# Performance work log

Hardware: AMD Instinct MI355X
Metric: run time of the kernel (lower is better)

## Reference

```python
import jax, jax.numpy as jnp
import numpy as np

WS = 3          # window_size == patch size (asserted in the torch forward)
R = WS // 2
V = WS ** 3     # 27 voxels per patch == window length
D_MODEL = 256
HEADS = 8
LAYERS = 3

_IDX = np.arange(WS)[:, None] + np.arange(WS)[None, :]  # [WS, WS] sliding-window indices into padded grid


def _layer_norm(x, g, b, eps=1e-5):
    mu = jnp.mean(x, axis=-1, keepdims=True)
    var = jnp.var(x, axis=-1, keepdims=True)
    return (x - mu) * jax.lax.rsqrt(var + eps) * g + b


def _gather_windows(x):
    # x: [B, WS, WS, WS, C] -> zero-padded 3x3x3 neighborhoods, [B*V, V, C]
    xp = jnp.pad(x, ((0, 0), (R, R), (R, R), (R, R), (0, 0)))
    nb = xp[:, _IDX][:, :, :, _IDX][:, :, :, :, :, _IDX]
    # axes: [B, d_ctr, d_win, h_ctr, h_win, w_ctr, w_win, C]
    nb = nb.transpose(0, 1, 3, 5, 2, 4, 6, 7)
    return nb.reshape(x.shape[0] * V, V, x.shape[-1])


def _window_mask(known_mask):
    # boundary (padding) positions -> False; interior -> known_mask value
    mp = jnp.pad(known_mask, ((0, 0), (R, R), (R, R), (R, R)))
    m = mp[:, _IDX][:, :, :, _IDX][:, :, :, :, :, _IDX]
    m = m.transpose(0, 1, 3, 5, 2, 4, 6)
    return m.reshape(known_mask.shape[0] * V, V)


def _forward(neighbors_patch, known_mask, w_in, b_in, pos_embed,
             ln1_g, ln1_b, ln2_g, ln2_b,
             Wq, bq, Wk, bk, Wv, bv, Wo, bo,
             W1, b1, W2, b2, w_out, b_out):
    B = neighbors_patch.shape[0]
    d = w_in.shape[0]
    hd = d // HEADS
    scale = hd ** -0.5
    # Conv3d(1, d, kernel_size=1) == per-voxel affine scalar -> d channels; then +pos_embed
    x = neighbors_patch[:, 0, :, :, :, None] * w_in + b_in + pos_embed  # [B,WS,WS,WS,d]
    mask = _window_mask(known_mask)  # [B*V, V] (constant across layers)
    N = B * V
    t = x.reshape(N, d)
    for l in range(LAYERS):
        # NOTE: K/V come from RAW (un-normed) neighbor embeddings, Q from norm1(target) - as in the torch code
        nb = _gather_windows(t.reshape(B, WS, WS, WS, d))  # [N, V, d]
        tn = _layer_norm(t, ln1_g[l], ln1_b[l])
        q = (tn @ Wq[l] + bq[l]).reshape(N, HEADS, hd)
        k = (nb @ Wk[l] + bk[l]).reshape(N, V, HEADS, hd)
        v = (nb @ Wv[l] + bv[l]).reshape(N, V, HEADS, hd)
        s = jnp.einsum('nhd,nlhd->nhl', q, k) * scale
        s = jnp.where(mask[:, None, :], s, -1e30)
        # fully-masked rows: torch softmax gives NaN then zeroed; here uniform*mask -> 0, same result
        a = jax.nn.softmax(s, axis=-1) * mask[:, None, :]
        o = jnp.einsum('nhl,nlhd->nhd', a, v).reshape(N, d) @ Wo[l] + bo[l]
        t = t + o  # dropout is identity in eval
        tn2 = _layer_norm(t, ln2_g[l], ln2_b[l])
        h = jax.nn.gelu(tn2 @ W1[l] + b1[l], approximate=False)
        t = t + h @ W2[l] + b2[l]
    center = t.reshape(B, WS, WS, WS, d)[:, R, R, R, :]
    return (center @ w_out)[:, None] + b_out  # [B, 1]


def setup_inputs():
    key = jax.random.key(0)
    ks = jax.random.split(key, 24)
    B, d, L, ff = 256, D_MODEL, LAYERS, 4 * D_MODEL
    nrm = lambda k, shape, s=0.02: jax.random.normal(k, shape, jnp.float32) * s
    return {
        'neighbors_patch': (jax.random.uniform(ks[0], (B, 1, WS, WS, WS)) < 0.5).astype(jnp.float32),
        'known_mask': jax.random.randint(ks[1], (B, WS, WS, WS), 0, 2).astype(bool),
        'w_in': nrm(ks[2], (d,), 0.5), 'b_in': nrm(ks[3], (d,)),
        'pos_embed': nrm(ks[4], (WS, WS, WS, d)),
        'ln1_g': jnp.ones((L, d)), 'ln1_b': jnp.zeros((L, d)),
        'ln2_g': jnp.ones((L, d)), 'ln2_b': jnp.zeros((L, d)),
        'Wq': nrm(ks[5], (L, d, d)), 'bq': nrm(ks[6], (L, d)),
        'Wk': nrm(ks[7], (L, d, d)), 'bk': nrm(ks[8], (L, d)),
        'Wv': nrm(ks[9], (L, d, d)), 'bv': nrm(ks[10], (L, d)),
        'Wo': nrm(ks[11], (L, d, d)), 'bo': nrm(ks[12], (L, d)),
        'W1': nrm(ks[13], (L, d, ff)), 'b1': nrm(ks[14], (L, ff)),
        'W2': nrm(ks[15], (L, ff, d)), 'b2': nrm(ks[16], (L, d)),
        'w_out': nrm(ks[17], (d,)), 'b_out': nrm(ks[18], (1,)),
    }


def reference(neighbors_patch, known_mask, w_in, b_in, pos_embed, ln1_g, ln1_b, ln2_g, ln2_b, Wq, bq, Wk, bk, Wv, bv, Wo, bo, W1, b1, W2, b2, w_out, b_out):
    return _forward(neighbors_patch, known_mask, w_in, b_in, pos_embed, ln1_g, ln1_b, ln2_g, ln2_b, Wq, bq, Wk, bk, Wv, bv, Wo, bo, W1, b1, W2, b2, w_out, b_out)
```

## Files before the change

kernel.cpp:

```cpp
#include <hip/hip_runtime.h>
#include <hip/hip_bf16.h>


#define NTOK 6912
#define DM   256
#define FF   1024

typedef __hip_bfloat16 bf16;
typedef __bf16 bf16x8 __attribute__((ext_vector_type(8)));
typedef float  f32x4  __attribute__((ext_vector_type(4)));

__device__ __forceinline__ void gload_lds16(const void* g, void* l) {
    __builtin_amdgcn_global_load_lds(
        (const __attribute__((address_space(1))) void*)g,
        (__attribute__((address_space(3))) void*)l, 16, 0, 0);
}

__device__ __forceinline__ unsigned short f2bf_bits(float x) {
    bf16 h = __float2bfloat16(x);
    union { bf16 h; unsigned short u; } c; c.h = h; return c.u;
}

__global__ __launch_bounds__(256) void embed_kernel(
    const float* __restrict__ npat, const float* __restrict__ w_in,
    const float* __restrict__ b_in, const float* __restrict__ pos,
    float* __restrict__ t, bf16* __restrict__ t_bf)
{
    int n = blockIdx.x;
    int c = threadIdx.x;
    int p = n % 27;
    float v = npat[n] * w_in[c] + b_in[c] + pos[p * DM + c];
    t[(size_t)n * DM + c] = v;
    t_bf[(size_t)n * DM + c] = __float2bfloat16(v);
}

__global__ void make_mask_kernel(const int* __restrict__ km,
                                 unsigned int* __restrict__ mask27)
{
    int n = blockIdx.x * blockDim.x + threadIdx.x;
    if (n >= NTOK) return;
    int b = n / 27, q = n % 27;
    int zq = q / 9, yq = (q / 3) % 3, xq = q % 3;
    unsigned int mb = 0u;
    for (int m = 0; m < 27; ++m) {
        int zm = m / 9, ym = (m / 3) % 3, xm = m % 3;
        if (abs(zm - zq) <= 1 && abs(ym - yq) <= 1 && abs(xm - xq) <= 1 &&
            km[b * 27 + m] != 0)
            mb |= (1u << m);
    }
    mask27[n] = mb;
}

__global__ __launch_bounds__(256) void convert_weights(
    const float* __restrict__ Wq, const float* __restrict__ Wk,
    const float* __restrict__ Wv, const float* __restrict__ Wo,
    const float* __restrict__ W1, const float* __restrict__ W2,
    bf16* __restrict__ Wt)
{
    __shared__ float tile[32][33];
    int id = blockIdx.z;
    int l = id / 6, wsel = id % 6;
    const float* src; bf16* dst; int K, N;
    if (wsel < 4) {
        const float* tbl[4] = {Wq, Wk, Wv, Wo};
        src = tbl[wsel] + (size_t)l * 65536; K = 256; N = 256;
        dst = Wt + (size_t)l * 786432 + wsel * 65536;
    } else if (wsel == 4) {
        src = W1 + (size_t)l * 262144; K = 256; N = 1024;
        dst = Wt + (size_t)l * 786432 + 262144;
    } else {
        src = W2 + (size_t)l * 262144; K = 1024; N = 256;
        dst = Wt + (size_t)l * 786432 + 524288;
    }
    int n0 = blockIdx.x * 32, k0 = blockIdx.y * 32;
    if (n0 >= N || k0 >= K) return;
    int tx = threadIdx.x, ty = threadIdx.y;
#pragma unroll
    for (int i = 0; i < 4; ++i)
        tile[ty + i * 8][tx] = src[(size_t)(k0 + ty + i * 8) * N + n0 + tx];
    __syncthreads();
#pragma unroll
    for (int i = 0; i < 4; ++i)
        dst[(size_t)(n0 + ty + i * 8) * K + k0 + tx] =
            __float2bfloat16(tile[tx][ty + i * 8]);
}

__global__ __launch_bounds__(256) void layernorm_kernel(
    const float* __restrict__ X, const float* __restrict__ g,
    const float* __restrict__ bta, bf16* __restrict__ Y)
{
    int n = blockIdx.x;
    int c = threadIdx.x;
    float x = X[(size_t)n * DM + c];
    float s = x, s2 = x * x;
    for (int off = 32; off; off >>= 1) {
        s  += __shfl_xor(s, off);
        s2 += __shfl_xor(s2, off);
    }
    __shared__ float ps[4], ps2[4];
    int w = c >> 6;
    if ((c & 63) == 0) { ps[w] = s; ps2[w] = s2; }
    __syncthreads();
    s  = ps[0] + ps[1] + ps[2] + ps[3];
    s2 = ps2[0] + ps2[1] + ps2[2] + ps2[3];
    float mu  = s * (1.0f / DM);
    float var = s2 * (1.0f / DM) - mu * mu;
    float r = rsqrtf(var + 1e-5f);
    Y[(size_t)n * DM + c] = __float2bfloat16((x - mu) * r * g[c] + bta[c]);
}

__device__ __forceinline__ void gemm_body(
    const bf16* __restrict__ A, const bf16* __restrict__ Bt,
    const float* __restrict__ bias, const float* __restrict__ residual,
    float* __restrict__ Cf, bf16* __restrict__ Cb,
    int K, int Nc, int act, int mode, int row0, int col0,
    bf16* As, bf16* Bs)
{
    int tid = threadIdx.x;
    int wv = tid >> 6, ln = tid & 63;
    int wr = wv >> 1, wc = wv & 1;

    f32x4 acc[4][2];
#pragma unroll
    for (int m = 0; m < 4; ++m)
#pragma unroll
        for (int n = 0; n < 2; ++n) acc[m][n] = (f32x4){0.f, 0.f, 0.f, 0.f};

    int lrow = ln >> 3;
    int kof  = (ln & 7) * 8;

    for (int k0 = 0; k0 < K; k0 += 64) {
        __syncthreads();
#pragma unroll
        for (int i = 0; i < 4; ++i) {
            int slot = i * 4 + wv;
            gload_lds16(A + (size_t)(row0 + slot * 8 + lrow) * K + k0 + kof,
                        As + slot * 512);
        }
#pragma unroll
        for (int i = 0; i < 2; ++i) {
            int slot = i * 4 + wv;
            gload_lds16(Bt + (size_t)(col0 + slot * 8 + lrow) * K + k0 + kof,
                        Bs + slot * 512);
        }
        __syncthreads();
        int lr = ln & 15, kg = ln >> 4;
#pragma unroll
        for (int kk = 0; kk < 2; ++kk) {
            int koff = kk * 32 + kg * 8;
            bf16x8 a[4], b[2];
#pragma unroll
            for (int m = 0; m < 4; ++m)
                a[m] = *(const bf16x8*)&As[(wr * 64 + m * 16 + lr) * 64 + koff];
#pragma unroll
            for (int n = 0; n < 2; ++n)
                b[n] = *(const bf16x8*)&Bs[(wc * 32 + n * 16 + lr) * 64 + koff];
#pragma unroll
            for (int m = 0; m < 4; ++m)
#pragma unroll
                for (int n = 0; n < 2; ++n)
                    acc[m][n] = __builtin_amdgcn_mfma_f32_16x16x32_bf16(
                        a[m], b[n], acc[m][n], 0, 0, 0);
        }
    }

    int lr = ln & 15, rg = ln >> 4;
#pragma unroll
    for (int m = 0; m < 4; ++m) {
#pragma unroll
        for (int n = 0; n < 2; ++n) {
            int col = col0 + wc * 32 + n * 16 + lr;
            float bcol = bias[col];
#pragma unroll
            for (int r = 0; r < 4; ++r) {
                int row = row0 + wr * 64 + m * 16 + rg * 4 + r;
                float v = acc[m][n][r] + bcol;
                if (mode == 2) {
                    int bb = row / 27, tok = row - bb * 27;
                    Cb[((size_t)bb * DM + col) * 32 + tok] = __float2bfloat16(v);
                } else {
                    size_t idx = (size_t)row * Nc + col;
                    if (residual) v += residual[idx];
                    if (act) v = 0.5f * v * (1.0f + erff(v * 0.70710678118654752f));
                    if (Cf) Cf[idx] = v;
                    if (Cb) Cb[idx] = __float2bfloat16(v);
                }
            }
        }
    }
}

__global__ __launch_bounds__(256) void gemm_bf16(
    const bf16* __restrict__ A, const bf16* __restrict__ Bt,
    const float* __restrict__ bias, const float* __restrict__ residual,
    float* __restrict__ Cf, bf16* __restrict__ Cb,
    int K, int Nc, int act)
{
    __shared__ __align__(16) bf16 As[128 * 64];
    __shared__ __align__(16) bf16 Bs[64 * 64];
    gemm_body(A, Bt, bias, residual, Cf, Cb, K, Nc, act, 0,
              blockIdx.x * 128, blockIdx.y * 64, As, Bs);
}

__global__ __launch_bounds__(256) void qkv_gemm(
    const bf16* __restrict__ tn, const bf16* __restrict__ tb,
    const bf16* __restrict__ wq,
    const float* __restrict__ bq, const float* __restrict__ bk,
    const float* __restrict__ bv,
    bf16* __restrict__ Qb, bf16* __restrict__ Kb, bf16* __restrict__ Vt)
{
    __shared__ __align__(16) bf16 As[128 * 64];
    __shared__ __align__(16) bf16 Bs[64 * 64];
    int ysel = blockIdx.y >> 2, ycol = blockIdx.y & 3;
    const bf16* A = (ysel == 0) ? tn : tb;
    const bf16* W = wq + (size_t)ysel * 65536;
    const float* bias = (ysel == 0) ? bq : (ysel == 1) ? bk : bv;
    bf16* Out = (ysel == 0) ? Qb : (ysel == 1) ? Kb : Vt;
    int mode = (ysel == 2) ? 2 : 0;
    gemm_body(A, W, bias, nullptr, nullptr, Out, DM, DM, 0, mode,
              blockIdx.x * 128, ycol * 64, As, Bs);
}

__global__ __launch_bounds__(256) void attention_mfma(
    const bf16* __restrict__ Qb, const bf16* __restrict__ Kb,
    const bf16* __restrict__ Vt, const unsigned int* __restrict__ mask27,
    bf16* __restrict__ out)
{
    __shared__ __align__(16) bf16 P_lds[4][32 * 40];
    int b  = blockIdx.x;
    int wv = threadIdx.x >> 6;
    int head = blockIdx.y * 4 + wv;
    int ln = threadIdx.x & 63;
    int r = ln & 15, g = ln >> 4;

    const bf16* Kp = Kb + (size_t)b * 27 * DM + head * 32;
    const bf16* Qp = Qb + (size_t)b * 27 * DM + head * 32;

    bf16x8 aK[2], bQ[2];
    aK[0] = *(const bf16x8*)(Kp + (size_t)r * DM + g * 8);
    aK[1] = *(const bf16x8*)(Kp + (size_t)(16 + r) * DM + g * 8);
    bQ[0] = *(const bf16x8*)(Qp + (size_t)r * DM + g * 8);
    bQ[1] = *(const bf16x8*)(Qp + (size_t)(16 + r) * DM + g * 8);

    f32x4 acc[2][2];
#pragma unroll
    for (int at = 0; at < 2; ++at)
#pragma unroll
        for (int bt = 0; bt < 2; ++bt)
            acc[at][bt] = __builtin_amdgcn_mfma_f32_16x16x32_bf16(
                aK[at], bQ[bt], (f32x4){0.f, 0.f, 0.f, 0.f}, 0, 0, 0);

    unsigned int Mq[2];
    Mq[0] = mask27[b * 27 + r];
    Mq[1] = (16 + r < 27) ? mask27[b * 27 + 16 + r] : 0u;

#pragma unroll
    for (int bt = 0; bt < 2; ++bt) {
        float e[2][4];
        float mx = -1e30f;
#pragma unroll
        for (int at = 0; at < 2; ++at)
#pragma unroll
            for (int rg = 0; rg < 4; ++rg) {
                int m = at * 16 + g * 4 + rg;
                bool in = (Mq[bt] >> m) & 1;
                float sv = acc[at][bt][rg] * 0.17677669529663687f;
                e[at][rg] = in ? sv : -1e30f;
                mx = fmaxf(mx, e[at][rg]);
            }
        mx = fmaxf(mx, __shfl_xor(mx, 16));
        mx = fmaxf(mx, __shfl_xor(mx, 32));
        float sum = 0.f;
#pragma unroll
        for (int at = 0; at < 2; ++at)
#pragma unroll
            for (int rg = 0; rg < 4; ++rg) {
                int m = at * 16 + g * 4 + rg;
                bool in = (Mq[bt] >> m) & 1;
                float ev = in ? expf(e[at][rg] - mx) : 0.f;
                e[at][rg] = ev;
                sum += ev;
            }
        sum += __shfl_xor(sum, 16);
        sum += __shfl_xor(sum, 32);
        float inv = (sum > 0.f) ? 1.f / sum : 0.f;
#pragma unroll
        for (int at = 0; at < 2; ++at) {
            ushort4 u;
            u.x = f2bf_bits(e[at][0] * inv);
            u.y = f2bf_bits(e[at][1] * inv);
            u.z = f2bf_bits(e[at][2] * inv);
            u.w = f2bf_bits(e[at][3] * inv);
            *(ushort4*)&P_lds[wv][(bt * 16 + r) * 40 + at * 16 + g * 4] = u;
        }
    }

    bf16x8 pa[2], vb[2];
    pa[0] = *(const bf16x8*)&P_lds[wv][(size_t)r * 40 + g * 8];
    pa[1] = *(const bf16x8*)&P_lds[wv][(size_t)(16 + r) * 40 + g * 8];
    const bf16* Vp = Vt + ((size_t)b * DM + head * 32) * 32;
    vb[0] = *(const bf16x8*)(Vp + (size_t)r * 32 + g * 8);
    vb[1] = *(const bf16x8*)(Vp + (size_t)(16 + r) * 32 + g * 8);

    f32x4 o[2][2];
#pragma unroll
    for (int qt = 0; qt < 2; ++qt)
#pragma unroll
        for (int dt = 0; dt < 2; ++dt)
            o[qt][dt] = __builtin_amdgcn_mfma_f32_16x16x32_bf16(
                pa[qt], vb[dt], (f32x4){0.f, 0.f, 0.f, 0.f}, 0, 0, 0);

#pragma unroll
    for (int qt = 0; qt < 2; ++qt)
#pragma unroll
        for (int dt = 0; dt < 2; ++dt)
#pragma unroll
            for (int rg = 0; rg < 4; ++rg) {
                int q = qt * 16 + g * 4 + rg;
                if (q < 27)
                    out[(size_t)(b * 27 + q) * DM + head * 32 + dt * 16 + r] =
                        __float2bfloat16(o[qt][dt][rg]);
            }
}

__global__ __launch_bounds__(256) void out_proj_kernel(
    const float* __restrict__ t, const float* __restrict__ w_out,
    const float* __restrict__ b_out, float* __restrict__ out)
{
    int bb = blockIdx.x;
    int c = threadIdx.x;
    float v = t[(size_t)(bb * 27 + 13) * DM + c] * w_out[c];
    for (int off = 32; off; off >>= 1) v += __shfl_xor(v, off);
    __shared__ float ps[4];
    if ((c & 63) == 0) ps[c >> 6] = v;
    __syncthreads();
    if (c == 0) out[bb] = ps[0] + ps[1] + ps[2] + ps[3] + b_out[0];
}

extern "C" void kernel_launch(void* const* d_in, const int* in_sizes, int n_in,
                              void* d_out, int out_size, void* d_ws, size_t ws_size,
                              hipStream_t stream)
{
    const float* npat  = (const float*)d_in[0];
    const int*   kmask = (const int*)  d_in[1];
    const float* w_in  = (const float*)d_in[2];
    const float* b_in  = (const float*)d_in[3];
    const float* pos   = (const float*)d_in[4];
    const float* ln1_g = (const float*)d_in[5];
    const float* ln1_b = (const float*)d_in[6];
    const float* ln2_g = (const float*)d_in[7];
    const float* ln2_b = (const float*)d_in[8];
    const float* Wq    = (const float*)d_in[9];
    const float* bq    = (const float*)d_in[10];
    const float* Wk    = (const float*)d_in[11];
    const float* bk    = (const float*)d_in[12];
    const float* Wv    = (const float*)d_in[13];
    const float* bv    = (const float*)d_in[14];
    const float* Wo    = (const float*)d_in[15];
    const float* bo    = (const float*)d_in[16];
    const float* W1    = (const float*)d_in[17];
    const float* b1    = (const float*)d_in[18];
    const float* W2    = (const float*)d_in[19];
    const float* b2    = (const float*)d_in[20];
    const float* w_out = (const float*)d_in[21];
    const float* b_out = (const float*)d_in[22];
    float* out = (float*)d_out;

    char* ws = (char*)d_ws;
    size_t f32mat = (size_t)NTOK * DM * 4;
    size_t bfmat  = (size_t)NTOK * DM * 2;
    float* t = (float*)(ws);
    char* p = ws + f32mat;
    bf16* t_bf   = (bf16*)(p);               p += bfmat;
    bf16* tn_bf  = (bf16*)(p);               p += bfmat;
    bf16* attn_bf= (bf16*)(p);               p += bfmat;
    bf16* Qb     = (bf16*)(p);               p += bfmat;
    bf16* Kb     = (bf16*)(p);               p += bfmat;
    bf16* Vt     = (bf16*)(p);               p += (size_t)256 * DM * 32 * 2;
    bf16* H_bf   = (bf16*)(p);               p += (size_t)NTOK * FF * 2;
    bf16* Wt     = (bf16*)(p);               p += (size_t)3 * 786432 * 2;
    unsigned int* mask27 = (unsigned int*)(p);

    convert_weights<<<dim3(32, 32, 18), dim3(32, 8), 0, stream>>>(
        Wq, Wk, Wv, Wo, W1, W2, Wt);
    embed_kernel<<<NTOK, 256, 0, stream>>>(npat, w_in, b_in, pos, t, t_bf);
    make_mask_kernel<<<(NTOK + 255) / 256, 256, 0, stream>>>(kmask, mask27);

    dim3 gDD(NTOK / 128, DM / 64);
    dim3 gQKV(NTOK / 128, 12);
    dim3 gFF(NTOK / 128, FF / 64);

    for (int l = 0; l < 3; ++l) {
        const bf16* wqt = Wt + (size_t)l * 786432;
        const bf16* wot = wqt + 3 * 65536;
        const bf16* w1t = wot + 65536;
        const bf16* w2t = w1t + 262144;

        layernorm_kernel<<<NTOK, 256, 0, stream>>>(t, ln1_g + l * DM, ln1_b + l * DM, tn_bf);
        qkv_gemm<<<gQKV, 256, 0, stream>>>(tn_bf, t_bf, wqt,
                                           bq + l * DM, bk + l * DM, bv + l * DM,
                                           Qb, Kb, Vt);
        attention_mfma<<<dim3(256, 2), 256, 0, stream>>>(Qb, Kb, Vt, mask27, attn_bf);
        gemm_bf16<<<gDD, 256, 0, stream>>>(attn_bf, wot, bo + l * DM, t, t, t_bf, DM, DM, 0);
        layernorm_kernel<<<NTOK, 256, 0, stream>>>(t, ln2_g + l * DM, ln2_b + l * DM, tn_bf);
        gemm_bf16<<<gFF, 256, 0, stream>>>(tn_bf, w1t, b1 + l * FF, nullptr, nullptr, H_bf, DM, FF, 1);
        gemm_bf16<<<gDD, 256, 0, stream>>>(H_bf, w2t, b2 + l * DM, t, t, t_bf, FF, DM, 0);
    }

    out_proj_kernel<<<256, 256, 0, stream>>>(t, w_out, b_out, out);
}
```

Before: 391.4 us.

## Double-buffer GEMM LDS tiles and fuse mask construction into embed kernel

```diff
diff --git a/kernel.cpp b/kernel.cpp
--- a/kernel.cpp
+++ b/kernel.cpp
@@ -21,34 +21,30 @@
     union { bf16 h; unsigned short u; } c; c.h = h; return c.u;
 }
 
-__global__ __launch_bounds__(256) void embed_kernel(
-    const float* __restrict__ npat, const float* __restrict__ w_in,
-    const float* __restrict__ b_in, const float* __restrict__ pos,
-    float* __restrict__ t, bf16* __restrict__ t_bf)
+__global__ __launch_bounds__(256) void embed_mask_kernel(
+    const float* __restrict__ npat, const int* __restrict__ km,
+    const float* __restrict__ w_in, const float* __restrict__ b_in,
+    const float* __restrict__ pos,
+    float* __restrict__ t, bf16* __restrict__ t_bf,
+    unsigned int* __restrict__ mask27)
 {
     int n = blockIdx.x;
     int c = threadIdx.x;
-    int p = n % 27;
-    float v = npat[n] * w_in[c] + b_in[c] + pos[p * DM + c];
+    int b = n / 27, q = n % 27;
+    float v = npat[n] * w_in[c] + b_in[c] + pos[q * DM + c];
     t[(size_t)n * DM + c] = v;
     t_bf[(size_t)n * DM + c] = __float2bfloat16(v);
-}
-
-__global__ void make_mask_kernel(const int* __restrict__ km,
-                                 unsigned int* __restrict__ mask27)
-{
-    int n = blockIdx.x * blockDim.x + threadIdx.x;
-    if (n >= NTOK) return;
-    int b = n / 27, q = n % 27;
-    int zq = q / 9, yq = (q / 3) % 3, xq = q % 3;
-    unsigned int mb = 0u;
-    for (int m = 0; m < 27; ++m) {
-        int zm = m / 9, ym = (m / 3) % 3, xm = m % 3;
-        if (abs(zm - zq) <= 1 && abs(ym - yq) <= 1 && abs(xm - xq) <= 1 &&
-            km[b * 27 + m] != 0)
-            mb |= (1u << m);
-    }
-    mask27[n] = mb;
+    if (c < 64) {
+        bool bit = false;
+        if (c < 27) {
+            int zq = q / 9, yq = (q / 3) % 3, xq = q % 3;
+            int zm = c / 9, ym = (c / 3) % 3, xm = c % 3;
+            bit = (abs(zm - zq) <= 1) && (abs(ym - yq) <= 1) &&
+                  (abs(xm - xq) <= 1) && (km[b * 27 + c] != 0);
+        }
+        unsigned long long bm = __ballot(bit);
+        if (c == 0) mask27[n] = (unsigned int)(bm & 0x7FFFFFFULL);
+    }
 }
 
 __global__ __launch_bounds__(256) void convert_weights(
@@ -128,33 +124,52 @@
 
     int lrow = ln >> 3;
     int kof  = (ln & 7) * 8;
-
-    for (int k0 = 0; k0 < K; k0 += 64) {
-        __syncthreads();
-#pragma unroll
-        for (int i = 0; i < 4; ++i) {
-            int slot = i * 4 + wv;
-            gload_lds16(A + (size_t)(row0 + slot * 8 + lrow) * K + k0 + kof,
-                        As + slot * 512);
+    int NT = K >> 6;
+
+#pragma unroll
+    for (int i = 0; i < 4; ++i) {
+        int slot = i * 4 + wv;
+        gload_lds16(A + (size_t)(row0 + slot * 8 + lrow) * K + kof,
+                    As + slot * 512);
+    }
+#pragma unroll
+    for (int i = 0; i < 2; ++i) {
+        int slot = i * 4 + wv;
+        gload_lds16(Bt + (size_t)(col0 + slot * 8 + lrow) * K + kof,
+                    Bs + slot * 512);
+    }
+    __syncthreads();
+
+    int lr = ln & 15, kg = ln >> 4;
+    for (int t = 0; t < NT; ++t) {
+        if (t + 1 < NT) {
+            int nb = (t + 1) & 1;
+            int nk = (t + 1) << 6;
+#pragma unroll
+            for (int i = 0; i < 4; ++i) {
+                int slot = i * 4 + wv;
+                gload_lds16(A + (size_t)(row0 + slot * 8 + lrow) * K + nk + kof,
+                            As + nb * 8192 + slot * 512);
+            }
+#pragma unroll
+            for (int i = 0; i < 2; ++i) {
+                int slot = i * 4 + wv;
+                gload_lds16(Bt + (size_t)(col0 + slot * 8 + lrow) * K + nk + kof,
+                            Bs + nb * 4096 + slot * 512);
+            }
         }
-#pragma unroll
-        for (int i = 0; i < 2; ++i) {
-            int slot = i * 4 + wv;
-            gload_lds16(Bt + (size_t)(col0 + slot * 8 + lrow) * K + k0 + kof,
-                        Bs + slot * 512);
-        }
-        __syncthreads();
-        int lr = ln & 15, kg = ln >> 4;
+        const bf16* Ab = As + (t & 1) * 8192;
+        const bf16* Bb = Bs + (t & 1) * 4096;
 #pragma unroll
         for (int kk = 0; kk < 2; ++kk) {
             int koff = kk * 32 + kg * 8;
             bf16x8 a[4], b[2];
 #pragma unroll
             for (int m = 0; m < 4; ++m)
-                a[m] = *(const bf16x8*)&As[(wr * 64 + m * 16 + lr) * 64 + koff];
+                a[m] = *(const bf16x8*)&Ab[(wr * 64 + m * 16 + lr) * 64 + koff];
 #pragma unroll
             for (int n = 0; n < 2; ++n)
-                b[n] = *(const bf16x8*)&Bs[(wc * 32 + n * 16 + lr) * 64 + koff];
+                b[n] = *(const bf16x8*)&Bb[(wc * 32 + n * 16 + lr) * 64 + koff];
 #pragma unroll
             for (int m = 0; m < 4; ++m)
 #pragma unroll
@@ -162,9 +177,10 @@
                     acc[m][n] = __builtin_amdgcn_mfma_f32_16x16x32_bf16(
                         a[m], b[n], acc[m][n], 0, 0, 0);
         }
-    }
-
-    int lr = ln & 15, rg = ln >> 4;
+        __syncthreads();
+    }
+
+    int rg = ln >> 4;
 #pragma unroll
     for (int m = 0; m < 4; ++m) {
 #pragma unroll
@@ -196,8 +212,8 @@
     float* __restrict__ Cf, bf16* __restrict__ Cb,
     int K, int Nc, int act)
 {
-    __shared__ __align__(16) bf16 As[128 * 64];
-    __shared__ __align__(16) bf16 Bs[64 * 64];
+    __shared__ __align__(16) bf16 As[2 * 128 * 64];
+    __shared__ __align__(16) bf16 Bs[2 * 64 * 64];
     gemm_body(A, Bt, bias, residual, Cf, Cb, K, Nc, act, 0,
               blockIdx.x * 128, blockIdx.y * 64, As, Bs);
 }
@@ -209,8 +225,8 @@
     const float* __restrict__ bv,
     bf16* __restrict__ Qb, bf16* __restrict__ Kb, bf16* __restrict__ Vt)
 {
-    __shared__ __align__(16) bf16 As[128 * 64];
-    __shared__ __align__(16) bf16 Bs[64 * 64];
+    __shared__ __align__(16) bf16 As[2 * 128 * 64];
+    __shared__ __align__(16) bf16 Bs[2 * 64 * 64];
     int ysel = blockIdx.y >> 2, ycol = blockIdx.y & 3;
     const bf16* A = (ysel == 0) ? tn : tb;
     const bf16* W = wq + (size_t)ysel * 65536;
@@ -383,8 +399,8 @@
 
     convert_weights<<<dim3(32, 32, 18), dim3(32, 8), 0, stream>>>(
         Wq, Wk, Wv, Wo, W1, W2, Wt);
-    embed_kernel<<<NTOK, 256, 0, stream>>>(npat, w_in, b_in, pos, t, t_bf);
-    make_mask_kernel<<<(NTOK + 255) / 256, 256, 0, stream>>>(kmask, mask27);
+    embed_mask_kernel<<<NTOK, 256, 0, stream>>>(npat, kmask, w_in, b_in, pos,
+                                                t, t_bf, mask27);
 
     dim3 gDD(NTOK / 128, DM / 64);
     dim3 gQKV(NTOK / 128, 12);
```

New measurement: 408.1 us. 4.2% more time.

## Fuse whole transformer pipeline into one persistent kernel with grid barriers

Applied to the files above, without the earlier changes.

```diff
diff --git a/kernel.cpp b/kernel.cpp
--- a/kernel.cpp
+++ b/kernel.cpp
@@ -5,6 +5,7 @@
 #define NTOK 6912
 #define DM   256
 #define FF   1024
+#define NB   216
 
 typedef __hip_bfloat16 bf16;
 typedef __bf16 bf16x8 __attribute__((ext_vector_type(8)));
@@ -21,99 +22,120 @@
     union { bf16 h; unsigned short u; } c; c.h = h; return c.u;
 }
 
-__global__ __launch_bounds__(256) void embed_kernel(
-    const float* __restrict__ npat, const float* __restrict__ w_in,
-    const float* __restrict__ b_in, const float* __restrict__ pos,
-    float* __restrict__ t, bf16* __restrict__ t_bf)
-{
-    int n = blockIdx.x;
-    int c = threadIdx.x;
-    int p = n % 27;
-    float v = npat[n] * w_in[c] + b_in[c] + pos[p * DM + c];
-    t[(size_t)n * DM + c] = v;
-    t_bf[(size_t)n * DM + c] = __float2bfloat16(v);
-}
-
-__global__ void make_mask_kernel(const int* __restrict__ km,
-                                 unsigned int* __restrict__ mask27)
-{
-    int n = blockIdx.x * blockDim.x + threadIdx.x;
-    if (n >= NTOK) return;
-    int b = n / 27, q = n % 27;
-    int zq = q / 9, yq = (q / 3) % 3, xq = q % 3;
-    unsigned int mb = 0u;
-    for (int m = 0; m < 27; ++m) {
-        int zm = m / 9, ym = (m / 3) % 3, xm = m % 3;
-        if (abs(zm - zq) <= 1 && abs(ym - yq) <= 1 && abs(xm - xq) <= 1 &&
-            km[b * 27 + m] != 0)
-            mb |= (1u << m);
-    }
-    mask27[n] = mb;
-}
-
-__global__ __launch_bounds__(256) void convert_weights(
-    const float* __restrict__ Wq, const float* __restrict__ Wk,
-    const float* __restrict__ Wv, const float* __restrict__ Wo,
-    const float* __restrict__ W1, const float* __restrict__ W2,
-    bf16* __restrict__ Wt)
-{
-    __shared__ float tile[32][33];
-    int id = blockIdx.z;
-    int l = id / 6, wsel = id % 6;
-    const float* src; bf16* dst; int K, N;
-    if (wsel < 4) {
-        const float* tbl[4] = {Wq, Wk, Wv, Wo};
-        src = tbl[wsel] + (size_t)l * 65536; K = 256; N = 256;
-        dst = Wt + (size_t)l * 786432 + wsel * 65536;
-    } else if (wsel == 4) {
-        src = W1 + (size_t)l * 262144; K = 256; N = 1024;
-        dst = Wt + (size_t)l * 786432 + 262144;
-    } else {
-        src = W2 + (size_t)l * 262144; K = 1024; N = 256;
-        dst = Wt + (size_t)l * 786432 + 524288;
-    }
-    int n0 = blockIdx.x * 32, k0 = blockIdx.y * 32;
-    if (n0 >= N || k0 >= K) return;
-    int tx = threadIdx.x, ty = threadIdx.y;
-#pragma unroll
-    for (int i = 0; i < 4; ++i)
-        tile[ty + i * 8][tx] = src[(size_t)(k0 + ty + i * 8) * N + n0 + tx];
+__device__ __forceinline__ void gridbar(int* cnt, int target) {
+    __threadfence();
     __syncthreads();
-#pragma unroll
-    for (int i = 0; i < 4; ++i)
-        dst[(size_t)(n0 + ty + i * 8) * K + k0 + tx] =
-            __float2bfloat16(tile[tx][ty + i * 8]);
-}
-
-__global__ __launch_bounds__(256) void layernorm_kernel(
-    const float* __restrict__ X, const float* __restrict__ g,
-    const float* __restrict__ bta, bf16* __restrict__ Y)
-{
-    int n = blockIdx.x;
-    int c = threadIdx.x;
-    float x = X[(size_t)n * DM + c];
-    float s = x, s2 = x * x;
-    for (int off = 32; off; off >>= 1) {
-        s  += __shfl_xor(s, off);
-        s2 += __shfl_xor(s2, off);
-    }
-    __shared__ float ps[4], ps2[4];
-    int w = c >> 6;
-    if ((c & 63) == 0) { ps[w] = s; ps2[w] = s2; }
+    if (threadIdx.x == 0) {
+        atomicAdd(cnt, 1);
+        while (__hip_atomic_load(cnt, __ATOMIC_RELAXED,
+                                 __HIP_MEMORY_SCOPE_AGENT) < target)
+            __builtin_amdgcn_s_sleep(2);
+    }
     __syncthreads();
-    s  = ps[0] + ps[1] + ps[2] + ps[3];
-    s2 = ps2[0] + ps2[1] + ps2[2] + ps2[3];
-    float mu  = s * (1.0f / DM);
-    float var = s2 * (1.0f / DM) - mu * mu;
-    float r = rsqrtf(var + 1e-5f);
-    Y[(size_t)n * DM + c] = __float2bfloat16((x - mu) * r * g[c] + bta[c]);
-}
-
-__device__ __forceinline__ void gemm_body(
-    const bf16* __restrict__ A, const bf16* __restrict__ Bt,
-    const float* __restrict__ bias, const float* __restrict__ residual,
-    float* __restrict__ Cf, bf16* __restrict__ Cb,
-    int K, int Nc, int act, int mode, int row0, int col0,
+    __threadfence();
+}
+
+__device__ void convert_stage(
+    const float* Wq, const float* Wk, const float* Wv, const float* Wo,
+    const float* W1, const float* W2, bf16* Wt, float* tile, int bid)
+{
+    int tx = threadIdx.x & 31, ty = threadIdx.x >> 5;
+    for (int j = bid; j < 2304; j += NB) {
+        const float* src; bf16* dst; int K, N, n0, k0;
+        if (j < 768) {
+            int id = j >> 6, tt = j & 63;
+            int l = id >> 2, wsel = id & 3;
+            const float* tbl[4] = {Wq, Wk, Wv, Wo};
+            src = tbl[wsel] + (size_t)l * 65536;
+            dst = Wt + (size_t)l * 786432 + wsel * 65536;
+            K = 256; N = 256; n0 = (tt & 7) * 32; k0 = (tt >> 3) * 32;
+        } else {
+            int jb = j - 768, id = jb >> 8, tt = jb & 255;
+            int l = id >> 1;
+            if ((id & 1) == 0) {
+                src = W1 + (size_t)l * 262144;
+                dst = Wt + (size_t)l * 786432 + 262144;
+                K = 256; N = 1024; n0 = (tt & 31) * 32; k0 = (tt >> 5) * 32;
+            } else {
+                src = W2 + (size_t)l * 262144;
+                dst = Wt + (size_t)l * 786432 + 524288;
+                K = 1024; N = 256; n0 = (tt & 7) * 32; k0 = (tt >> 3) * 32;
+            }
+        }
+        __syncthreads();
+#pragma unroll
+        for (int i = 0; i < 4; ++i)
+            tile[(ty + i * 8) * 33 + tx] =
+                src[(size_t)(k0 + ty + i * 8) * N + n0 + tx];
+        __syncthreads();
+#pragma unroll
+        for (int i = 0; i < 4; ++i)
+            dst[(size_t)(n0 + ty + i * 8) * K + k0 + tx] =
+                __float2bfloat16(tile[tx * 33 + ty + i * 8]);
+    }
+}
+
+__device__ void embed_stage(
+    const float* npat, const int* km, const float* w_in, const float* b_in,
+    const float* pos, float* t, bf16* t_bf, unsigned int* mask27, int bid)
+{
+    int wv = threadIdx.x >> 6, ln = threadIdx.x & 63;
+    float4 w4 = *(const float4*)&w_in[ln * 4];
+    float4 bi4 = *(const float4*)&b_in[ln * 4];
+    for (int i = 0; i < 8; ++i) {
+        int n = bid * 32 + wv * 8 + i;
+        int b = n / 27, q = n - b * 27;
+        float nv = npat[n];
+        float4 p4 = *(const float4*)&pos[q * DM + ln * 4];
+        float4 v;
+        v.x = nv * w4.x + bi4.x + p4.x;  v.y = nv * w4.y + bi4.y + p4.y;
+        v.z = nv * w4.z + bi4.z + p4.z;  v.w = nv * w4.w + bi4.w + p4.w;
+        *(float4*)&t[(size_t)n * DM + ln * 4] = v;
+        ushort4 o;
+        o.x = f2bf_bits(v.x); o.y = f2bf_bits(v.y);
+        o.z = f2bf_bits(v.z); o.w = f2bf_bits(v.w);
+        *(ushort4*)&t_bf[(size_t)n * DM + ln * 4] = o;
+        bool bit = false;
+        if (ln < 27) {
+            int zq = q / 9, yq = (q / 3) % 3, xq = q % 3;
+            int zm = ln / 9, ym = (ln / 3) % 3, xm = ln % 3;
+            bit = (abs(zm - zq) <= 1) && (abs(ym - yq) <= 1) &&
+                  (abs(xm - xq) <= 1) && (km[b * 27 + ln] != 0);
+        }
+        unsigned long long bm = __ballot(bit);
+        if (ln == 0) mask27[n] = (unsigned int)(bm & 0x7FFFFFFULL);
+    }
+}
+
+__device__ void ln_stage(const float* X, const float* g, const float* bta,
+                         bf16* Y, int bid)
+{
+    int wv = threadIdx.x >> 6, ln = threadIdx.x & 63;
+    float4 g4 = *(const float4*)&g[ln * 4];
+    float4 b4 = *(const float4*)&bta[ln * 4];
+    for (int i = 0; i < 8; ++i) {
+        int n = bid * 32 + wv * 8 + i;
+        float4 x4 = *(const float4*)&X[(size_t)n * DM + ln * 4];
+        float s = x4.x + x4.y + x4.z + x4.w;
+        float s2 = x4.x * x4.x + x4.y * x4.y + x4.z * x4.z + x4.w * x4.w;
+        for (int off = 32; off; off >>= 1) {
+            s += __shfl_xor(s, off); s2 += __shfl_xor(s2, off);
+        }
+        float mu = s * (1.0f / DM);
+        float var = s2 * (1.0f / DM) - mu * mu;
+        float r = rsqrtf(var + 1e-5f);
+        ushort4 o;
+        o.x = f2bf_bits((x4.x - mu) * r * g4.x + b4.x);
+        o.y = f2bf_bits((x4.y - mu) * r * g4.y + b4.y);
+        o.z = f2bf_bits((x4.z - mu) * r * g4.z + b4.z);
+        o.w = f2bf_bits((x4.w - mu) * r * g4.w + b4.w);
+        *(ushort4*)&Y[(size_t)n * DM + ln * 4] = o;
+    }
+}
+
+__device__ void gemm_tile(
+    const bf16* A, const bf16* Bt, const float* bias, const float* residual,
+    float* Cf, bf16* Cb, int K, int Nc, int act, int mode, int row0, int col0,
     bf16* As, bf16* Bs)
 {
     int tid = threadIdx.x;
@@ -190,48 +212,15 @@
     }
 }
 
-__global__ __launch_bounds__(256) void gemm_bf16(
-    const bf16* __restrict__ A, const bf16* __restrict__ Bt,
-    const float* __restrict__ bias, const float* __restrict__ residual,
-    float* __restrict__ Cf, bf16* __restrict__ Cb,
-    int K, int Nc, int act)
-{
-    __shared__ __align__(16) bf16 As[128 * 64];
-    __shared__ __align__(16) bf16 Bs[64 * 64];
-    gemm_body(A, Bt, bias, residual, Cf, Cb, K, Nc, act, 0,
-              blockIdx.x * 128, blockIdx.y * 64, As, Bs);
-}
-
-__global__ __launch_bounds__(256) void qkv_gemm(
-    const bf16* __restrict__ tn, const bf16* __restrict__ tb,
-    const bf16* __restrict__ wq,
-    const float* __restrict__ bq, const float* __restrict__ bk,
-    const float* __restrict__ bv,
-    bf16* __restrict__ Qb, bf16* __restrict__ Kb, bf16* __restrict__ Vt)
-{
-    __shared__ __align__(16) bf16 As[128 * 64];
-    __shared__ __align__(16) bf16 Bs[64 * 64];
-    int ysel = blockIdx.y >> 2, ycol = blockIdx.y & 3;
-    const bf16* A = (ysel == 0) ? tn : tb;
-    const bf16* W = wq + (size_t)ysel * 65536;
-    const float* bias = (ysel == 0) ? bq : (ysel == 1) ? bk : bv;
-    bf16* Out = (ysel == 0) ? Qb : (ysel == 1) ? Kb : Vt;
-    int mode = (ysel == 2) ? 2 : 0;
-    gemm_body(A, W, bias, nullptr, nullptr, Out, DM, DM, 0, mode,
-              blockIdx.x * 128, ycol * 64, As, Bs);
-}
-
-__global__ __launch_bounds__(256) void attention_mfma(
-    const bf16* __restrict__ Qb, const bf16* __restrict__ Kb,
-    const bf16* __restrict__ Vt, const unsigned int* __restrict__ mask27,
-    bf16* __restrict__ out)
-{
-    __shared__ __align__(16) bf16 P_lds[4][32 * 40];
-    int b  = blockIdx.x;
+__device__ void attn_patch(
+    const bf16* Qb, const bf16* Kb, const bf16* Vt,
+    const unsigned int* mask27, bf16* out, int b, int y, bf16* Pbase)
+{
     int wv = threadIdx.x >> 6;
-    int head = blockIdx.y * 4 + wv;
+    int head = y * 4 + wv;
     int ln = threadIdx.x & 63;
     int r = ln & 15, g = ln >> 4;
+    bf16* P = Pbase + wv * 1280;
 
     const bf16* Kp = Kb + (size_t)b * 27 * DM + head * 32;
     const bf16* Qp = Qb + (size_t)b * 27 * DM + head * 32;
@@ -291,13 +280,13 @@
             u.y = f2bf_bits(e[at][1] * inv);
             u.z = f2bf_bits(e[at][2] * inv);
             u.w = f2bf_bits(e[at][3] * inv);
-            *(ushort4*)&P_lds[wv][(bt * 16 + r) * 40 + at * 16 + g * 4] = u;
+            *(ushort4*)&P[(bt * 16 + r) * 40 + at * 16 + g * 4] = u;
         }
     }
 
     bf16x8 pa[2], vb[2];
-    pa[0] = *(const bf16x8*)&P_lds[wv][(size_t)r * 40 + g * 8];
-    pa[1] = *(const bf16x8*)&P_lds[wv][(size_t)(16 + r) * 40 + g * 8];
+    pa[0] = *(const bf16x8*)&P[(size_t)r * 40 + g * 8];
+    pa[1] = *(const bf16x8*)&P[(size_t)(16 + r) * 40 + g * 8];
     const bf16* Vp = Vt + ((size_t)b * DM + head * 32) * 32;
     vb[0] = *(const bf16x8*)(Vp + (size_t)r * 32 + g * 8);
     vb[1] = *(const bf16x8*)(Vp + (size_t)(16 + r) * 32 + g * 8);
@@ -323,18 +312,95 @@
             }
 }
 
-__global__ __launch_bounds__(256) void out_proj_kernel(
-    const float* __restrict__ t, const float* __restrict__ w_out,
-    const float* __restrict__ b_out, float* __restrict__ out)
-{
-    int bb = blockIdx.x;
-    int c = threadIdx.x;
-    float v = t[(size_t)(bb * 27 + 13) * DM + c] * w_out[c];
-    for (int off = 32; off; off >>= 1) v += __shfl_xor(v, off);
-    __shared__ float ps[4];
-    if ((c & 63) == 0) ps[c >> 6] = v;
-    __syncthreads();
-    if (c == 0) out[bb] = ps[0] + ps[1] + ps[2] + ps[3] + b_out[0];
+__global__ void init_bar(int* bar) { if (threadIdx.x == 0) bar[0] = 0; }
+
+__global__ __launch_bounds__(256) void mega(
+    const float* __restrict__ npat, const int* __restrict__ km,
+    const float* __restrict__ w_in, const float* __restrict__ b_in,
+    const float* __restrict__ pos,
+    const float* __restrict__ ln1_g, const float* __restrict__ ln1_b,
+    const float* __restrict__ ln2_g, const float* __restrict__ ln2_b,
+    const float* __restrict__ Wq, const float* __restrict__ bq,
+    const float* __restrict__ Wk, const float* __restrict__ bk,
+    const float* __restrict__ Wv, const float* __restrict__ bv,
+    const float* __restrict__ Wo, const float* __restrict__ bo,
+    const float* __restrict__ W1, const float* __restrict__ b1,
+    const float* __restrict__ W2, const float* __restrict__ b2,
+    const float* __restrict__ w_out, const float* __restrict__ b_out,
+    float* __restrict__ out,
+    int* bar, float* t, bf16* t_bf, bf16* tn_bf, bf16* attn_bf,
+    bf16* Qb, bf16* Kb, bf16* Vt, bf16* H_bf, bf16* Wt,
+    unsigned int* mask27)
+{
+    __shared__ __align__(16) char smem[24576];
+    bf16* As = (bf16*)smem;
+    bf16* Bs = (bf16*)(smem + 16384);
+    int bid = blockIdx.x;
+    int epoch = 0;
+#define BAR() do { ++epoch; gridbar(bar, epoch * NB); } while (0)
+
+    convert_stage(Wq, Wk, Wv, Wo, W1, W2, Wt, (float*)smem, bid);
+    embed_stage(npat, km, w_in, b_in, pos, t, t_bf, mask27, bid);
+    BAR();
+
+    int bx = bid % 54, ycol = bid / 54;
+
+    for (int l = 0; l < 3; ++l) {
+        const bf16* wqt = Wt + (size_t)l * 786432;
+        const bf16* wkt = wqt + 65536;
+        const bf16* wvt = wkt + 65536;
+        const bf16* wot = wvt + 65536;
+        const bf16* w1t = wot + 65536;
+        const bf16* w2t = w1t + 262144;
+
+        ln_stage(t, ln1_g + l * DM, ln1_b + l * DM, tn_bf, bid);
+        BAR();
+
+        gemm_tile(tn_bf, wqt, bq + l * DM, nullptr, nullptr, Qb,
+                  256, 256, 0, 0, bx * 128, ycol * 64, As, Bs);
+        gemm_tile(t_bf,  wkt, bk + l * DM, nullptr, nullptr, Kb,
+                  256, 256, 0, 0, bx * 128, ycol * 64, As, Bs);
+        gemm_tile(t_bf,  wvt, bv + l * DM, nullptr, nullptr, Vt,
+                  256, 256, 0, 2, bx * 128, ycol * 64, As, Bs);
+        BAR();
+
+        for (int p = bid; p < 256; p += NB)
+            for (int y = 0; y < 2; ++y)
+                attn_patch(Qb, Kb, Vt, mask27, attn_bf, p, y, (bf16*)smem);
+        BAR();
+
+        gemm_tile(attn_bf, wot, bo + l * DM, t, t, t_bf,
+                  256, 256, 0, 0, bx * 128, ycol * 64, As, Bs);
+        BAR();
+
+        ln_stage(t, ln2_g + l * DM, ln2_b + l * DM, tn_bf, bid);
+        BAR();
+
+        for (int i = 0; i < 4; ++i) {
+            int vb = i * NB + bid;
+            int fx = vb % 54, fy = vb / 54;
+            gemm_tile(tn_bf, w1t, b1 + l * FF, nullptr, nullptr, H_bf,
+                      256, 1024, 1, 0, fx * 128, fy * 64, As, Bs);
+        }
+        BAR();
+
+        gemm_tile(H_bf, w2t, b2 + l * DM, t, t, t_bf,
+                  1024, 256, 0, 0, bx * 128, ycol * 64, As, Bs);
+        BAR();
+    }
+
+    {
+        int wv = threadIdx.x >> 6, ln = threadIdx.x & 63;
+        int b = wv * NB + bid;
+        if (b < 256) {
+            float4 x4 = *(const float4*)&t[(size_t)(b * 27 + 13) * DM + ln * 4];
+            float4 w4 = *(const float4*)&w_out[ln * 4];
+            float v = x4.x * w4.x + x4.y * w4.y + x4.z * w4.z + x4.w * w4.w;
+            for (int off = 32; off; off >>= 1) v += __shfl_xor(v, off);
+            if (ln == 0) out[b] = v + b_out[0];
+        }
+    }
+#undef BAR
 }
 
 extern "C" void kernel_launch(void* const* d_in, const int* in_sizes, int n_in,
@@ -367,45 +433,22 @@
     float* out = (float*)d_out;
 
     char* ws = (char*)d_ws;
-    size_t f32mat = (size_t)NTOK * DM * 4;
-    size_t bfmat  = (size_t)NTOK * DM * 2;
-    float* t = (float*)(ws);
-    char* p = ws + f32mat;
-    bf16* t_bf   = (bf16*)(p);               p += bfmat;
-    bf16* tn_bf  = (bf16*)(p);               p += bfmat;
-    bf16* attn_bf= (bf16*)(p);               p += bfmat;
-    bf16* Qb     = (bf16*)(p);               p += bfmat;
-    bf16* Kb     = (bf16*)(p);               p += bfmat;
-    bf16* Vt     = (bf16*)(p);               p += (size_t)256 * DM * 32 * 2;
-    bf16* H_bf   = (bf16*)(p);               p += (size_t)NTOK * FF * 2;
-    bf16* Wt     = (bf16*)(p);               p += (size_t)3 * 786432 * 2;
-    unsigned int* mask27 = (unsigned int*)(p);
-
-    convert_weights<<<dim3(32, 32, 18), dim3(32, 8), 0, stream>>>(
-        Wq, Wk, Wv, Wo, W1, W2, Wt);
-    embed_kernel<<<NTOK, 256, 0, stream>>>(npat, w_in, b_in, pos, t, t_bf);
-    make_mask_kernel<<<(NTOK + 255) / 256, 256, 0, stream>>>(kmask, mask27);
-
-    dim3 gDD(NTOK / 128, DM / 64);
-    dim3 gQKV(NTOK / 128, 12);
-    dim3 gFF(NTOK / 128, FF / 64);
-
-    for (int l = 0; l < 3; ++l) {
-        const bf16* wqt = Wt + (size_t)l * 786432;
-        const bf16* wot = wqt + 3 * 65536;
-        const bf16* w1t = wot + 65536;
-        const bf16* w2t = w1t + 262144;
-
-        layernorm_kernel<<<NTOK, 256, 0, stream>>>(t, ln1_g + l * DM, ln1_b + l * DM, tn_bf);
-        qkv_gemm<<<gQKV, 256, 0, stream>>>(tn_bf, t_bf, wqt,
-                                           bq + l * DM, bk + l * DM, bv + l * DM,
-                                           Qb, Kb, Vt);
-        attention_mfma<<<dim3(256, 2), 256, 0, stream>>>(Qb, Kb, Vt, mask27, attn_bf);
-        gemm_bf16<<<gDD, 256, 0, stream>>>(attn_bf, wot, bo + l * DM, t, t, t_bf, DM, DM, 0);
-        layernorm_kernel<<<NTOK, 256, 0, stream>>>(t, ln2_g + l * DM, ln2_b + l * DM, tn_bf);
-        gemm_bf16<<<gFF, 256, 0, stream>>>(tn_bf, w1t, b1 + l * FF, nullptr, nullptr, H_bf, DM, FF, 1);
-        gemm_bf16<<<gDD, 256, 0, stream>>>(H_bf, w2t, b2 + l * DM, t, t, t_bf, FF, DM, 0);
-    }
-
-    out_proj_kernel<<<256, 256, 0, stream>>>(t, w_out, b_out, out);
-}
+    int* bar = (int*)ws;
+    char* p = ws + 256;
+    float* t = (float*)p;                    p += (size_t)NTOK * DM * 4;
+    bf16* t_bf    = (bf16*)p;                p += (size_t)NTOK * DM * 2;
+    bf16* tn_bf   = (bf16*)p;                p += (size_t)NTOK * DM * 2;
+    bf16* attn_bf = (bf16*)p;                p += (size_t)NTOK * DM * 2;
+    bf16* Qb      = (bf16*)p;                p += (size_t)NTOK * DM * 2;
+    bf16* Kb      = (bf16*)p;                p += (size_t)NTOK * DM * 2;
+    bf16* Vt      = (bf16*)p;                p += (size_t)256 * DM * 32 * 2;
+    bf16* H_bf    = (bf16*)p;                p += (size_t)NTOK * FF * 2;
+    bf16* Wt      = (bf16*)p;                p += (size_t)3 * 786432 * 2;
+    unsigned int* mask27 = (unsigned int*)p;
+
+    init_bar<<<1, 64, 0, stream>>>(bar);
+    mega<<<NB, 256, 0, stream>>>(
+        npat, kmask, w_in, b_in, pos, ln1_g, ln1_b, ln2_g, ln2_b,
+        Wq, bq, Wk, bk, Wv, bv, Wo, bo, W1, b1, W2, b2, w_out, b_out, out,
+        bar, t, t_bf, tn_bf, attn_bf, Qb, Kb, Vt, H_bf, Wt, mask27);
+}
```

Result: slower. 1.358 ms (+247.0%).
